# Kernel optimization log

Hardware: AMD Instinct MI355X
Metric: run time of the kernel (lower is better)

The kernel has to match this reference:

```python
import jax, jax.numpy as jnp
import numpy as np

# ---- static config (mirrors init_kwargs) ----
EMBED_DIM = 128
NUM_HEADS = 4
N_SUB = 16       # token grid is N_SUB x N_SUB, seq = N_SUB**2
WINDOW = 4
SHIFT = 2
EPS = 1e-5
NEG_INF = -1e9


def _swin_mask(n_sub, ws, shift):
    """Standard Swin attention mask for shifted windows. [NW, T, T]."""
    img = np.zeros((n_sub, n_sub), np.int32)
    cnt = 0
    for hs in (slice(0, -ws), slice(-ws, -shift), slice(-shift, None)):
        for wsl in (slice(0, -ws), slice(-ws, -shift), slice(-shift, None)):
            img[hs, wsl] = cnt
            cnt += 1
    nw = n_sub // ws
    ids = img.reshape(nw, ws, nw, ws).transpose(0, 2, 1, 3).reshape(nw * nw, ws * ws)
    mask = np.where(ids[:, None, :] != ids[:, :, None], NEG_INF, 0.0).astype(np.float32)
    return jnp.asarray(mask)


MASK = _swin_mask(N_SUB, WINDOW, SHIFT)


def _inorm(v):
    # InstanceNorm2d (affine=False) over spatial dims, per (batch, seq, channel)
    m = v.mean(axis=(-2, -1), keepdims=True)
    var = v.var(axis=(-2, -1), keepdims=True)
    return (v - m) * jax.lax.rsqrt(var + EPS)


def _pw(x, w, b):
    # pointwise (1x1) linear over channel dim of [..., C, H, W]
    return jnp.einsum('...chw,cd->...dhw', x, w) + b[:, None, None]


def _window(x, nw, ws):
    # [B, n_sub, n_sub, C, H, W] -> [B, nw*nw, ws*ws, C, H, W]
    B = x.shape[0]
    C, H, W = x.shape[3:]
    x = x.reshape(B, nw, ws, nw, ws, C, H, W)
    return x.transpose(0, 1, 3, 2, 4, 5, 6, 7).reshape(B, nw * nw, ws * ws, C, H, W)


def _unwindow(x, nw, ws):
    B = x.shape[0]
    C, H, W = x.shape[3:]
    x = x.reshape(B, nw, nw, ws, ws, C, H, W)
    return x.transpose(0, 1, 3, 2, 4, 5, 6, 7).reshape(B, nw * ws, nw * ws, C, H, W)


def _swin_func_attn(v, w_q, b_q, w_k, b_k, w_v, b_v, w_o, b_o):
    B, S, C, H, W = v.shape
    nw = N_SUB // WINDOW
    g = v.reshape(B, N_SUB, N_SUB, C, H, W)
    if SHIFT > 0:
        g = jnp.roll(g, (-SHIFT, -SHIFT), axis=(1, 2))
    q = _window(_pw(g, w_q, b_q), nw, WINDOW)
    k = _window(_pw(g, w_k, b_k), nw, WINDOW)
    val = _window(_pw(g, w_v, b_v), nw, WINDOW)
    d = C // NUM_HEADS
    T = WINDOW * WINDOW
    split = lambda x: x.reshape(B, nw * nw, T, NUM_HEADS, d, H, W)
    q, k, val = split(q), split(k), split(val)
    # integral score: spatial mean of per-head dot products, scaled by sqrt(d)
    scale = 1.0 / (np.sqrt(d) * H * W)
    scores = jnp.einsum('bnthdxy,bnshdxy->bnhts', q, k) * scale
    scores = scores + MASK[None, :, None, :, :]
    attn = jax.nn.softmax(scores, axis=-1)
    o = jnp.einsum('bnhts,bnshdxy->bnthdxy', attn, val)
    o = o.reshape(B, nw * nw, T, C, H, W)
    o = _pw(o, w_o, b_o)
    o = _unwindow(o, nw, WINDOW)
    if SHIFT > 0:
        o = jnp.roll(o, (SHIFT, SHIFT), axis=(1, 2))
    return o.reshape(B, S, C, H, W)


def _mlp(x, w1, b1, w2, b2):
    return _pw(jax.nn.gelu(_pw(x, w1, b1)), w2, b2)


def setup_inputs() -> dict:
    key = jax.random.key(0)
    ks = jax.random.split(key, 8)
    B, S, C, H, W = 8, N_SUB * N_SUB, EMBED_DIM, 16, 16
    p = 0.02
    return {
        'v': jax.random.normal(ks[0], (B, S, C, H, W), jnp.float32),
        'w_q': jax.random.normal(ks[1], (C, C), jnp.float32) * p,
        'b_q': jnp.zeros((C,), jnp.float32),
        'w_k': jax.random.normal(ks[2], (C, C), jnp.float32) * p,
        'b_k': jnp.zeros((C,), jnp.float32),
        'w_v': jax.random.normal(ks[3], (C, C), jnp.float32) * p,
        'b_v': jnp.zeros((C,), jnp.float32),
        'w_o': jax.random.normal(ks[4], (C, C), jnp.float32) * p,
        'b_o': jnp.zeros((C,), jnp.float32),
        'w1': jax.random.normal(ks[5], (C, C), jnp.float32) * p,
        'b1': jnp.zeros((C,), jnp.float32),
        'w2': jax.random.normal(ks[6], (C, C), jnp.float32) * p,
        'b2': jnp.zeros((C,), jnp.float32),
    }


def reference(v, w_q, b_q, w_k, b_k, w_v, b_v, w_o, b_o, w1, b1, w2, b2):
    v = _swin_func_attn(_inorm(v), w_q, b_q, w_k, b_k, w_v, b_v, w_o, b_o) + v
    v = _mlp(_inorm(v), w1, b1, w2, b2) + v
    return v
```

## Files before the change

### kernel.cpp

```cpp
#include <hip/hip_runtime.h>
#include <cstdint>
#include <cstddef>

#define DI __device__ __forceinline__

typedef unsigned short u16;
typedef u16 u16x8 __attribute__((ext_vector_type(8)));
typedef u16 u16x4 __attribute__((ext_vector_type(4)));
typedef float f32x4 __attribute__((ext_vector_type(4)));
typedef __bf16 bf16x8 __attribute__((ext_vector_type(8)));

constexpr float EPSf  = 1e-5f;
constexpr float SCALE = 1.0f / (5.656854249492381f * 256.0f);

DI float bf2f(u16 u) { union { uint32_t i; float f; } v; v.i = ((uint32_t)u) << 16; return v.f; }
DI u16 f2bf(float f) {
    union { float f; uint32_t i; } v; v.f = f;
    uint32_t r = v.i + 0x7fffu + ((v.i >> 16) & 1u);
    return (u16)(r >> 16);
}
DI bf16x8 u2b(u16x8 u) { union { u16x8 a; bf16x8 b; } v; v.a = u; return v.b; }

DI f32x4 MFMA(bf16x8 a, bf16x8 b, f32x4 c) {
    return __builtin_amdgcn_mfma_f32_16x16x32_bf16(a, b, c, 0, 0, 0);
}

DI int region3(int x) { return x < 12 ? 0 : (x < 14 ? 1 : 2); }

DI float gelu_f(float x) {
    float u = 1.5957691216f * x * (1.f + 0.044715f * x * x);
    return x * __builtin_amdgcn_rcpf(1.f + __expf(-u));
}

__global__ __launch_bounds__(256) void kw_prep(
        const float* __restrict__ w_q, const float* __restrict__ w_k,
        const float* __restrict__ w_v, const float* __restrict__ w_o,
        const float* __restrict__ w1,  const float* __restrict__ w2,
        u16* __restrict__ wt) {
    __shared__ float lds[128 * 129];
    const float* W;
    switch (blockIdx.x) {
        case 0: W = w_q; break; case 1: W = w_k; break; case 2: W = w_v; break;
        case 3: W = w_o; break; case 4: W = w1;  break; default: W = w2;  break;
    }
    u16* O = wt + blockIdx.x * 16384;
    int tid = threadIdx.x;
    for (int i = 0; i < 16; i++) {
        int flat = i * 1024 + tid * 4;
        float4 vv = *(const float4*)(W + flat);
        int c = flat >> 7, d = flat & 127;
        lds[c * 129 + d + 0] = vv.x; lds[c * 129 + d + 1] = vv.y;
        lds[c * 129 + d + 2] = vv.z; lds[c * 129 + d + 3] = vv.w;
    }
    __syncthreads();
    for (int i = 0; i < 32; i++) {
        int flat2 = i * 512 + tid * 2;
        int d = flat2 >> 7, c = flat2 & 127;
        u16 a = f2bf(lds[c * 129 + d]);
        u16 b = f2bf(lds[(c + 1) * 129 + d]);
        uint32_t pk = (uint32_t)a | ((uint32_t)b << 16);
        *(uint32_t*)(O + flat2) = pk;
    }
}

__global__ __launch_bounds__(512, 4) void k2_qkv(
        const float* __restrict__ v, const u16* __restrict__ wt,
        const float* __restrict__ b_q, const float* __restrict__ b_k,
        const float* __restrict__ b_v,
        u16* __restrict__ Qg, u16* __restrict__ Kg, u16* __restrict__ Vg) {
    __shared__ __align__(16) u16 Raw[34816];
    __shared__ float red[2][4][128];
    __shared__ float stats[2][128];

    int tid = threadIdx.x;
    int wtk = blockIdx.x;
    int b = wtk >> 8, n = (wtk >> 4) & 15, t = wtk & 15;
    int wi = n >> 2, wj = n & 3, ti = t >> 2, tj = t & 3;
    int si = (wi * 4 + ti + 2) & 15, sj = (wj * 4 + tj + 2) & 15;
    const float* src = v + (size_t)(b * 256 + si * 16 + sj) * 32768;

    int wave = tid >> 6, lane = tid & 63;

    #pragma unroll
    for (int i = 0; i < 16; i++) {
        int c = i * 8 + wave;
        float4 f = *(const float4*)(src + c * 256 + lane * 4);
        u16x4 u; u.x = f2bf(f.x); u.y = f2bf(f.y); u.z = f2bf(f.z); u.w = f2bf(f.w);
        *(u16x4*)&Raw[c * 268 + lane * 4] = u;
    }
    __syncthreads();
    {
        int c = tid & 127, p = tid >> 7;
        float s = 0.f, q = 0.f;
        #pragma unroll
        for (int k = 0; k < 16; k++) {
            u16x4 u = *(const u16x4*)&Raw[c * 268 + p * 64 + k * 4];
            float x0 = bf2f(u.x), x1 = bf2f(u.y), x2 = bf2f(u.z), x3 = bf2f(u.w);
            s += x0 + x1 + x2 + x3;
            q += x0 * x0 + x1 * x1 + x2 * x2 + x3 * x3;
        }
        red[0][p][c] = s; red[1][p][c] = q;
    }
    __syncthreads();
    if (tid < 128) {
        int c = tid;
        float s = red[0][0][c] + red[0][1][c] + red[0][2][c] + red[0][3][c];
        float q = red[1][0][c] + red[1][1][c] + red[1][2][c] + red[1][3][c];
        float mean = s * (1.f / 256.f);
        float var = q * (1.f / 256.f) - mean * mean;
        float a = rsqrtf(var + EPSf);
        stats[0][c] = a; stats[1][c] = -mean * a;
    }
    __syncthreads();

    int lrow = lane & 15, quad = lane >> 4;
    bf16x8 afr[2][4];
    #pragma unroll
    for (int kt = 0; kt < 4; kt++) {
        float sa[8], sb[8];
        #pragma unroll
        for (int j = 0; j < 8; j++) {
            int c = kt * 32 + quad * 8 + j;
            sa[j] = stats[0][c]; sb[j] = stats[1][c];
        }
        #pragma unroll
        for (int mi = 0; mi < 2; mi++) {
            int xy = (wave * 2 + mi) * 16 + lrow;
            u16x8 o;
            #pragma unroll
            for (int j = 0; j < 8; j++) {
                int c = kt * 32 + quad * 8 + j;
                o[j] = f2bf(fmaf(bf2f(Raw[c * 268 + xy]), sa[j], sb[j]));
            }
            afr[mi][kt] = u2b(o);
        }
    }
    __syncthreads();

    u16* WTs  = Raw;
    u16* stgw = Raw + 17408 + wave * 2176;
    for (int w = 0; w < 3; w++) {
        const u16* WTp = wt + w * 16384;
        const float* bias = (w == 0) ? b_q : (w == 1) ? b_k : b_v;
        u16* O = ((w == 0) ? Qg : (w == 1) ? Kg : Vg) + (size_t)wtk * 32768;
        if (w) __syncthreads();
        #pragma unroll
        for (int i = 0; i < 4; i++) {
            int flat = i * 4096 + tid * 8;
            *(u16x8*)&WTs[(flat >> 7) * 136 + (flat & 127)] =
                *(const u16x8*)&WTp[flat];
        }
        __syncthreads();
        f32x4 acc[2][8];
        #pragma unroll
        for (int mi = 0; mi < 2; mi++)
            #pragma unroll
            for (int nt = 0; nt < 8; nt++) acc[mi][nt] = (f32x4){0.f, 0.f, 0.f, 0.f};
        #pragma unroll
        for (int kt = 0; kt < 4; kt++) {
            #pragma unroll
            for (int nt = 0; nt < 8; nt++) {
                bf16x8 bfr = *(const bf16x8*)&WTs[(nt * 16 + lrow) * 136 + kt * 32 + quad * 8];
                acc[0][nt] = MFMA(afr[0][kt], bfr, acc[0][nt]);
                acc[1][nt] = MFMA(afr[1][kt], bfr, acc[1][nt]);
            }
        }
        #pragma unroll
        for (int mi = 0; mi < 2; mi++) {
            int mt = wave * 2 + mi;
            #pragma unroll
            for (int nt = 0; nt < 8; nt++) {
                int d = nt * 16 + lrow;
                float bv = bias[d];
                #pragma unroll
                for (int r = 0; r < 4; r++)
                    stgw[(quad * 4 + r) * 136 + d] = f2bf(acc[mi][nt][r] + bv);
            }
            #pragma unroll
            for (int ro = 0; ro < 4; ro++) {
                int flat = ro * 512 + lane * 8;
                *(u16x8*)&O[mt * 2048 + flat] =
                    *(const u16x8*)&stgw[(flat >> 7) * 136 + (flat & 127)];
            }
        }
    }
}

__global__ __launch_bounds__(1024, 4) void k3_scores(
        const u16* __restrict__ Qg, const u16* __restrict__ Kg,
        float* __restrict__ spart) {
    __shared__ f32x4 red3[3][4][64];
    int tid = threadIdx.x;
    int bid = blockIdx.x;
    int b = bid >> 5, n = (bid >> 1) & 15, half = bid & 1;
    int wtb = (b * 16 + n) * 16;
    int lane = tid & 63, wave = tid >> 6;
    int head = wave & 3, sub = wave >> 2;
    int lrow = lane & 15, quad = lane >> 4;
    int xyb = half * 128 + sub * 32;
    const u16* Qp = Qg + (size_t)(wtb + lrow) * 32768 + (size_t)xyb * 128 + head * 32 + quad * 8;
    const u16* Kp = Kg + (size_t)(wtb + lrow) * 32768 + (size_t)xyb * 128 + head * 32 + quad * 8;
    f32x4 acc = {0.f, 0.f, 0.f, 0.f};
    #pragma unroll 4
    for (int kt = 0; kt < 32; kt++) {
        bf16x8 aq = *(const bf16x8*)(Qp + kt * 128);
        bf16x8 bk = *(const bf16x8*)(Kp + kt * 128);
        acc = MFMA(aq, bk, acc);
    }
    if (sub) red3[sub - 1][head][lane] = acc;
    __syncthreads();
    if (sub == 0) {
        f32x4 a0 = red3[0][head][lane];
        f32x4 a1 = red3[1][head][lane];
        f32x4 a2 = red3[2][head][lane];
        acc = acc + a0 + a1 + a2;
        float* sp = spart + (size_t)(((half * 8 + b) * 16 + n) * 4 + head) * 256;
        for (int r = 0; r < 4; r++) sp[(quad * 4 + r) * 16 + lrow] = acc[r];
    }
}

__global__ __launch_bounds__(512, 4) void k4_attnout(
        const float* __restrict__ v, const u16* __restrict__ Vg,
        const float* __restrict__ spart, const u16* __restrict__ wt,
        const float* __restrict__ b_o, u16* __restrict__ v2) {
    __shared__ __align__(16) u16 Vc[32768];
    __shared__ float attn[4][16][16];
    int tid = threadIdx.x;
    int bid = blockIdx.x;
    int b = bid >> 6, n = (bid >> 2) & 15, qtr = bid & 3;
    int wi = n >> 2, wj = n & 3;
    int wtb = (b * 16 + n) * 16;

    if (tid < 64) {
        int h = tid >> 4, t = tid & 15;
        int it = wi * 4 + (t >> 2) , jt = wj * 4 + (t & 3);
        int rt = region3(it) * 3 + region3(jt);
        const float* sp0 = spart + (size_t)(((0 + b) * 16 + n) * 4 + h) * 256 + t * 16;
        const float* sp1 = spart + (size_t)(((8 + b) * 16 + n) * 4 + h) * 256 + t * 16;
        float vals[16]; float mx = -1e30f;
        for (int s = 0; s < 16; s++) {
            int is = wi * 4 + (s >> 2), js = wj * 4 + (s & 3);
            int rs = region3(is) * 3 + region3(js);
            float sc = (sp0[s] + sp1[s]) * SCALE + (rs == rt ? 0.f : -1e9f);
            vals[s] = sc; mx = fmaxf(mx, sc);
        }
        float sum = 0.f;
        for (int s = 0; s < 16; s++) { vals[s] = __expf(vals[s] - mx); sum += vals[s]; }
        float inv = 1.f / sum;
        for (int s = 0; s < 16; s++) attn[h][t][s] = vals[s] * inv;
    }
    __syncthreads();

    int lane = tid & 63, wave = tid >> 6;
    int lrow = lane & 15, quad = lane >> 4;
    const u16* WoT = wt + 3 * 16384;

    for (int sub = 0; sub < 4; sub++) {
        int xyb = qtr * 64 + sub * 16;
        if (sub) __syncthreads();
        #pragma unroll
        for (int it = 0; it < 8; it++) {
            int flat = (it * 512 + tid) * 8;
            int s = flat >> 11, rem = flat & 2047;
            int xyl = rem >> 7, ch = (rem & 127) >> 3;
            *(u16x8*)&Vc[s * 2048 + xyl * 128 + ((ch ^ (xyl & 7)) << 3)] =
                *(const u16x8*)&Vg[(size_t)(wtb + s) * 32768 + xyb * 128 + rem];
        }
        __syncthreads();
        bf16x8 pa[2][4];
        int t0 = wave * 2, t1 = wave * 2 + 1;
        #pragma unroll
        for (int kt = 0; kt < 4; kt++) {
            float oa[8], ob[8];
            #pragma unroll
            for (int j = 0; j < 8; j++) { oa[j] = 0.f; ob[j] = 0.f; }
            #pragma unroll
            for (int s = 0; s < 16; s++) {
                float a0 = attn[kt][t0][s], a1 = attn[kt][t1][s];
                u16x8 vv = *(const u16x8*)&Vc[s * 2048 + lrow * 128 +
                                              (((kt * 4 + quad) ^ (lrow & 7)) << 3)];
                #pragma unroll
                for (int j = 0; j < 8; j++) {
                    float x = bf2f(vv[j]);
                    oa[j] = fmaf(a0, x, oa[j]);
                    ob[j] = fmaf(a1, x, ob[j]);
                }
            }
            u16x8 ua, ub;
            #pragma unroll
            for (int j = 0; j < 8; j++) { ua[j] = f2bf(oa[j]); ub[j] = f2bf(ob[j]); }
            pa[0][kt] = u2b(ua); pa[1][kt] = u2b(ub);
        }
        __syncthreads();
        f32x4 acc[2][8];
        #pragma unroll
        for (int mi = 0; mi < 2; mi++)
            #pragma unroll
            for (int nt = 0; nt < 8; nt++) acc[mi][nt] = (f32x4){0.f, 0.f, 0.f, 0.f};
        #pragma unroll
        for (int kt = 0; kt < 4; kt++) {
            #pragma unroll
            for (int nt = 0; nt < 8; nt++) {
                bf16x8 bfr = *(const bf16x8*)&WoT[(nt * 16 + lrow) * 128 + kt * 32 + quad * 8];
                acc[0][nt] = MFMA(pa[0][kt], bfr, acc[0][nt]);
                acc[1][nt] = MFMA(pa[1][kt], bfr, acc[1][nt]);
            }
        }
        u16* stgw = Vc + wave * 2176;
        #pragma unroll
        for (int mi = 0; mi < 2; mi++) {
            int mt = wave * 2 + mi;
            int sd = (((wi * 4 + (mt >> 2) + 2) & 15) << 4) | ((wj * 4 + (mt & 3) + 2) & 15);
            size_t tokbase = (size_t)(b * 256 + sd) * 32768;
            #pragma unroll
            for (int nt = 0; nt < 8; nt++) {
                int cc = nt * 16 + lrow;
                float bv = b_o[cc];
                float4 res = *(const float4*)&v[tokbase + (size_t)cc * 256 + xyb + quad * 4];
                stgw[(quad * 4 + 0) * 136 + cc] = f2bf(acc[mi][nt][0] + bv + res.x);
                stgw[(quad * 4 + 1) * 136 + cc] = f2bf(acc[mi][nt][1] + bv + res.y);
                stgw[(quad * 4 + 2) * 136 + cc] = f2bf(acc[mi][nt][2] + bv + res.z);
                stgw[(quad * 4 + 3) * 136 + cc] = f2bf(acc[mi][nt][3] + bv + res.w);
            }
            size_t obase = tokbase + (size_t)xyb * 128;
            #pragma unroll
            for (int ro = 0; ro < 4; ro++) {
                int flat = ro * 512 + lane * 8;
                *(u16x8*)&v2[obase + flat] =
                    *(const u16x8*)&stgw[(flat >> 7) * 136 + (flat & 127)];
            }
        }
    }
}

__global__ __launch_bounds__(512, 4) void k6_mlp(
        const u16* __restrict__ v2, const u16* __restrict__ wt,
        const float* __restrict__ b1, const float* __restrict__ b2,
        float* __restrict__ out) {
    __shared__ __align__(16) u16 Nbuf[256 * 136];
    __shared__ __align__(16) u16 Hbuf[256 * 136];
    __shared__ float red[2][4][128];
    __shared__ float stats[2][128];
    int tid = threadIdx.x;
    size_t tok = blockIdx.x;
    const u16* src = v2 + tok * 32768;

    #pragma unroll
    for (int it = 0; it < 8; it++) {
        int flat = (it * 512 + tid) * 8;
        int xy = flat >> 7, c = flat & 127;
        *(u16x8*)&Nbuf[xy * 136 + c] = *(const u16x8*)&src[flat];
    }
    {
        const u16* W1T = wt + 4 * 16384;
        #pragma unroll
        for (int i = 0; i < 4; i++) {
            int flat = i * 4096 + tid * 8;
            *(u16x8*)&Hbuf[(flat >> 7) * 136 + (flat & 127)] = *(const u16x8*)&W1T[flat];
        }
    }
    __syncthreads();
    {
        int c = tid & 127, p = tid >> 7;
        float s = 0.f, q = 0.f;
        for (int k = 0; k < 64; k++) {
            float x = bf2f(Nbuf[(p * 64 + k) * 136 + c]);
            s += x; q += x * x;
        }
        red[0][p][c] = s; red[1][p][c] = q;
    }
    __syncthreads();
    if (tid < 128) {
        int c = tid;
        float s = red[0][0][c] + red[0][1][c] + red[0][2][c] + red[0][3][c];
        float q = red[1][0][c] + red[1][1][c] + red[1][2][c] + red[1][3][c];
        float mean = s * (1.f / 256.f);
        float var = q * (1.f / 256.f) - mean * mean;
        float a = rsqrtf(var + EPSf);
        stats[0][c] = a; stats[1][c] = -mean * a;
    }
    __syncthreads();

    int wave = tid >> 6, lane = tid & 63;
    int lrow = lane & 15, quad = lane >> 4;
    const u16* W2T = wt + 5 * 16384;

    {
        bf16x8 afr[2][4];
        #pragma unroll
        for (int kt = 0; kt < 4; kt++) {
            float sa[8], sb[8];
            #pragma unroll
            for (int j = 0; j < 8; j++) {
                int c = kt * 32 + quad * 8 + j;
                sa[j] = stats[0][c]; sb[j] = stats[1][c];
            }
            #pragma unroll
            for (int mi = 0; mi < 2; mi++) {
                int mt = wave * 2 + mi;
                u16x8 raw = *(const u16x8*)&Nbuf[(mt * 16 + lrow) * 136 + kt * 32 + quad * 8];
                u16x8 o;
                #pragma unroll
                for (int j = 0; j < 8; j++)
                    o[j] = f2bf(fmaf(bf2f(raw[j]), sa[j], sb[j]));
                afr[mi][kt] = u2b(o);
            }
        }
        f32x4 acc[2][8];
        #pragma unroll
        for (int mi = 0; mi < 2; mi++)
            #pragma unroll
            for (int nt = 0; nt < 8; nt++) acc[mi][nt] = (f32x4){0.f, 0.f, 0.f, 0.f};
        #pragma unroll
        for (int kt = 0; kt < 4; kt++) {
            #pragma unroll
            for (int nt = 0; nt < 8; nt++) {
                bf16x8 bfr = *(const bf16x8*)&Hbuf[(nt * 16 + lrow) * 136 + kt * 32 + quad * 8];
                acc[0][nt] = MFMA(afr[0][kt], bfr, acc[0][nt]);
                acc[1][nt] = MFMA(afr[1][kt], bfr, acc[1][nt]);
            }
        }
        __syncthreads();
        #pragma unroll
        for (int mi = 0; mi < 2; mi++) {
            int mt = wave * 2 + mi;
            #pragma unroll
            for (int nt = 0; nt < 8; nt++) {
                int c = nt * 16 + lrow;
                float bv = b1[c];
                #pragma unroll
                for (int r = 0; r < 4; r++) {
                    float x = acc[mi][nt][r] + bv;
                    Hbuf[(mt * 16 + quad * 4 + r) * 136 + c] = f2bf(gelu_f(x));
                }
            }
        }
    }
    {
        bf16x8 afr[2][4];
        #pragma unroll
        for (int mi = 0; mi < 2; mi++) {
            int mt = wave * 2 + mi;
            #pragma unroll
            for (int kt = 0; kt < 4; kt++)
                afr[mi][kt] = *(const bf16x8*)&Hbuf[(mt * 16 + lrow) * 136 + kt * 32 + quad * 8];
        }
        f32x4 acc[2][8];
        #pragma unroll
        for (int mi = 0; mi < 2; mi++)
            #pragma unroll
            for (int nt = 0; nt < 8; nt++) acc[mi][nt] = (f32x4){0.f, 0.f, 0.f, 0.f};
        #pragma unroll
        for (int kt = 0; kt < 4; kt++) {
            #pragma unroll
            for (int nt = 0; nt < 8; nt++) {
                bf16x8 bfr = *(const bf16x8*)&W2T[(nt * 16 + lrow) * 128 + kt * 32 + quad * 8];
                acc[0][nt] = MFMA(afr[0][kt], bfr, acc[0][nt]);
                acc[1][nt] = MFMA(afr[1][kt], bfr, acc[1][nt]);
            }
        }
        #pragma unroll
        for (int mi = 0; mi < 2; mi++) {
            int mt = wave * 2 + mi;
            #pragma unroll
            for (int nt = 0; nt < 8; nt++) {
                int c = nt * 16 + lrow;
                float bv = b2[c];
                f32x4 o4;
                #pragma unroll
                for (int r = 0; r < 4; r++) {
                    int m = mt * 16 + quad * 4 + r;
                    o4[r] = acc[mi][nt][r] + bv + bf2f(Nbuf[m * 136 + c]);
                }
                *(f32x4*)&out[tok * 32768 + (size_t)c * 256 + mt * 16 + quad * 4] = o4;
            }
        }
    }
}

extern "C" void kernel_launch(void* const* d_in, const int* in_sizes, int n_in,
                              void* d_out, int out_size, void* d_ws, size_t ws_size,
                              hipStream_t stream) {
    const float* v   = (const float*)d_in[0];
    const float* w_q = (const float*)d_in[1];
    const float* b_q = (const float*)d_in[2];
    const float* w_k = (const float*)d_in[3];
    const float* b_k = (const float*)d_in[4];
    const float* w_v = (const float*)d_in[5];
    const float* b_v = (const float*)d_in[6];
    const float* w_o = (const float*)d_in[7];
    const float* b_o = (const float*)d_in[8];
    const float* w1  = (const float*)d_in[9];
    const float* b1  = (const float*)d_in[10];
    const float* w2  = (const float*)d_in[11];
    const float* b2  = (const float*)d_in[12];

    u16*   wt    = (u16*)d_ws;
    float* spart = (float*)((char*)d_ws + 196608);
    u16*   Qg    = (u16*)((char*)d_ws + 1245184);
    u16*   v2    = Qg;
    u16*   Vg    = (u16*)d_out;
    u16*   Kg    = (u16*)d_out + 67108864;
    float* out   = (float*)d_out;

    kw_prep  <<<6,    256,  0, stream>>>(w_q, w_k, w_v, w_o, w1, w2, wt);
    k2_qkv   <<<2048, 512,  0, stream>>>(v, wt, b_q, b_k, b_v, Qg, Kg, Vg);
    k3_scores<<<256,  1024, 0, stream>>>(Qg, Kg, spart);
    k4_attnout<<<512, 512,  0, stream>>>(v, Vg, spart, wt, b_o, v2);
    k6_mlp   <<<2048, 512,  0, stream>>>(v2, wt, b1, b2, out);
}
```

Measured before the change: 1.232 ms.

## Read weights and V directly from global memory, drop LDS staging and syncs

The QKV projection now reads weight fragments straight from global memory instead of staging them in LDS behind barriers. The attention-output kernel loads V rows from global per thread, so the shared V cache and its barriers are gone. The MLP kernel drops its shared activation buffer: statistics come from a register-plus-shuffle reduction over direct global loads, and W1 is read from global. The output GEMMs loop over one M tile at a time to cut accumulator registers. This lowers LDS use and barriers so more blocks can run per CU, at the cost of more global and L2 traffic with less coalesced access.

```diff
diff --git a/kernel.cpp b/kernel.cpp
--- a/kernel.cpp
+++ b/kernel.cpp
@@ -137,20 +137,11 @@
     }
     __syncthreads();
 
-    u16* WTs  = Raw;
-    u16* stgw = Raw + 17408 + wave * 2176;
+    u16* stgw = Raw + wave * 2176;
     for (int w = 0; w < 3; w++) {
         const u16* WTp = wt + w * 16384;
         const float* bias = (w == 0) ? b_q : (w == 1) ? b_k : b_v;
         u16* O = ((w == 0) ? Qg : (w == 1) ? Kg : Vg) + (size_t)wtk * 32768;
-        if (w) __syncthreads();
-        #pragma unroll
-        for (int i = 0; i < 4; i++) {
-            int flat = i * 4096 + tid * 8;
-            *(u16x8*)&WTs[(flat >> 7) * 136 + (flat & 127)] =
-                *(const u16x8*)&WTp[flat];
-        }
-        __syncthreads();
         f32x4 acc[2][8];
         #pragma unroll
         for (int mi = 0; mi < 2; mi++)
@@ -160,7 +151,7 @@
         for (int kt = 0; kt < 4; kt++) {
             #pragma unroll
             for (int nt = 0; nt < 8; nt++) {
-                bf16x8 bfr = *(const bf16x8*)&WTs[(nt * 16 + lrow) * 136 + kt * 32 + quad * 8];
+                bf16x8 bfr = *(const bf16x8*)&WTp[(nt * 16 + lrow) * 128 + kt * 32 + quad * 8];
                 acc[0][nt] = MFMA(afr[0][kt], bfr, acc[0][nt]);
                 acc[1][nt] = MFMA(afr[1][kt], bfr, acc[1][nt]);
             }
@@ -223,8 +214,8 @@
         const float* __restrict__ v, const u16* __restrict__ Vg,
         const float* __restrict__ spart, const u16* __restrict__ wt,
         const float* __restrict__ b_o, u16* __restrict__ v2) {
-    __shared__ __align__(16) u16 Vc[32768];
     __shared__ float attn[4][16][16];
+    __shared__ __align__(16) u16 stg[8 * 2176];
     int tid = threadIdx.x;
     int bid = blockIdx.x;
     int b = bid >> 6, n = (bid >> 2) & 15, qtr = bid & 3;
@@ -254,21 +245,12 @@
     int lane = tid & 63, wave = tid >> 6;
     int lrow = lane & 15, quad = lane >> 4;
     const u16* WoT = wt + 3 * 16384;
+    u16* stgw = stg + wave * 2176;
+    int t0 = wave * 2, t1 = t0 + 1;
 
     for (int sub = 0; sub < 4; sub++) {
         int xyb = qtr * 64 + sub * 16;
-        if (sub) __syncthreads();
-        #pragma unroll
-        for (int it = 0; it < 8; it++) {
-            int flat = (it * 512 + tid) * 8;
-            int s = flat >> 11, rem = flat & 2047;
-            int xyl = rem >> 7, ch = (rem & 127) >> 3;
-            *(u16x8*)&Vc[s * 2048 + xyl * 128 + ((ch ^ (xyl & 7)) << 3)] =
-                *(const u16x8*)&Vg[(size_t)(wtb + s) * 32768 + xyb * 128 + rem];
-        }
-        __syncthreads();
         bf16x8 pa[2][4];
-        int t0 = wave * 2, t1 = wave * 2 + 1;
         #pragma unroll
         for (int kt = 0; kt < 4; kt++) {
             float oa[8], ob[8];
@@ -276,9 +258,9 @@
             for (int j = 0; j < 8; j++) { oa[j] = 0.f; ob[j] = 0.f; }
             #pragma unroll
             for (int s = 0; s < 16; s++) {
+                u16x8 vv = *(const u16x8*)&Vg[(size_t)(wtb + s) * 32768 +
+                                              (size_t)(xyb + lrow) * 128 + kt * 32 + quad * 8];
                 float a0 = attn[kt][t0][s], a1 = attn[kt][t1][s];
-                u16x8 vv = *(const u16x8*)&Vc[s * 2048 + lrow * 128 +
-                                              (((kt * 4 + quad) ^ (lrow & 7)) << 3)];
                 #pragma unroll
                 for (int j = 0; j < 8; j++) {
                     float x = bf2f(vv[j]);
@@ -291,24 +273,19 @@
             for (int j = 0; j < 8; j++) { ua[j] = f2bf(oa[j]); ub[j] = f2bf(ob[j]); }
             pa[0][kt] = u2b(ua); pa[1][kt] = u2b(ub);
         }
-        __syncthreads();
-        f32x4 acc[2][8];
-        #pragma unroll
-        for (int mi = 0; mi < 2; mi++)
-            #pragma unroll
-            for (int nt = 0; nt < 8; nt++) acc[mi][nt] = (f32x4){0.f, 0.f, 0.f, 0.f};
-        #pragma unroll
-        for (int kt = 0; kt < 4; kt++) {
-            #pragma unroll
-            for (int nt = 0; nt < 8; nt++) {
-                bf16x8 bfr = *(const bf16x8*)&WoT[(nt * 16 + lrow) * 128 + kt * 32 + quad * 8];
-                acc[0][nt] = MFMA(pa[0][kt], bfr, acc[0][nt]);
-                acc[1][nt] = MFMA(pa[1][kt], bfr, acc[1][nt]);
-            }
-        }
-        u16* stgw = Vc + wave * 2176;
         #pragma unroll
         for (int mi = 0; mi < 2; mi++) {
+            f32x4 acc[8];
+            #pragma unroll
+            for (int nt = 0; nt < 8; nt++) acc[nt] = (f32x4){0.f, 0.f, 0.f, 0.f};
+            #pragma unroll
+            for (int kt = 0; kt < 4; kt++) {
+                #pragma unroll
+                for (int nt = 0; nt < 8; nt++) {
+                    bf16x8 bfr = *(const bf16x8*)&WoT[(nt * 16 + lrow) * 128 + kt * 32 + quad * 8];
+                    acc[nt] = MFMA(pa[mi][kt], bfr, acc[nt]);
+                }
+            }
             int mt = wave * 2 + mi;
             int sd = (((wi * 4 + (mt >> 2) + 2) & 15) << 4) | ((wj * 4 + (mt & 3) + 2) & 15);
             size_t tokbase = (size_t)(b * 256 + sd) * 32768;
@@ -317,10 +294,10 @@
                 int cc = nt * 16 + lrow;
                 float bv = b_o[cc];
                 float4 res = *(const float4*)&v[tokbase + (size_t)cc * 256 + xyb + quad * 4];
-                stgw[(quad * 4 + 0) * 136 + cc] = f2bf(acc[mi][nt][0] + bv + res.x);
-                stgw[(quad * 4 + 1) * 136 + cc] = f2bf(acc[mi][nt][1] + bv + res.y);
-                stgw[(quad * 4 + 2) * 136 + cc] = f2bf(acc[mi][nt][2] + bv + res.z);
-                stgw[(quad * 4 + 3) * 136 + cc] = f2bf(acc[mi][nt][3] + bv + res.w);
+                stgw[(quad * 4 + 0) * 136 + cc] = f2bf(acc[nt][0] + bv + res.x);
+                stgw[(quad * 4 + 1) * 136 + cc] = f2bf(acc[nt][1] + bv + res.y);
+                stgw[(quad * 4 + 2) * 136 + cc] = f2bf(acc[nt][2] + bv + res.z);
+                stgw[(quad * 4 + 3) * 136 + cc] = f2bf(acc[nt][3] + bv + res.w);
             }
             size_t obase = tokbase + (size_t)xyb * 128;
             #pragma unroll
@@ -337,43 +314,46 @@
         const u16* __restrict__ v2, const u16* __restrict__ wt,
         const float* __restrict__ b1, const float* __restrict__ b2,
         float* __restrict__ out) {
-    __shared__ __align__(16) u16 Nbuf[256 * 136];
     __shared__ __align__(16) u16 Hbuf[256 * 136];
-    __shared__ float red[2][4][128];
+    __shared__ float red[2][8][128];
     __shared__ float stats[2][128];
     int tid = threadIdx.x;
     size_t tok = blockIdx.x;
     const u16* src = v2 + tok * 32768;
-
-    #pragma unroll
-    for (int it = 0; it < 8; it++) {
-        int flat = (it * 512 + tid) * 8;
-        int xy = flat >> 7, c = flat & 127;
-        *(u16x8*)&Nbuf[xy * 136 + c] = *(const u16x8*)&src[flat];
-    }
+    int wave = tid >> 6, lane = tid & 63;
+
     {
-        const u16* W1T = wt + 4 * 16384;
-        #pragma unroll
-        for (int i = 0; i < 4; i++) {
-            int flat = i * 4096 + tid * 8;
-            *(u16x8*)&Hbuf[(flat >> 7) * 136 + (flat & 127)] = *(const u16x8*)&W1T[flat];
-        }
-    }
-    __syncthreads();
-    {
-        int c = tid & 127, p = tid >> 7;
-        float s = 0.f, q = 0.f;
-        for (int k = 0; k < 64; k++) {
-            float x = bf2f(Nbuf[(p * 64 + k) * 136 + c]);
-            s += x; q += x * x;
-        }
-        red[0][p][c] = s; red[1][p][c] = q;
+        float s[8], q[8];
+        #pragma unroll
+        for (int j = 0; j < 8; j++) { s[j] = 0.f; q[j] = 0.f; }
+        #pragma unroll
+        for (int it = 0; it < 8; it++) {
+            u16x8 u = *(const u16x8*)&src[(it * 512 + tid) * 8];
+            #pragma unroll
+            for (int j = 0; j < 8; j++) {
+                float x = bf2f(u[j]);
+                s[j] += x; q[j] += x * x;
+            }
+        }
+        #pragma unroll
+        for (int j = 0; j < 8; j++) {
+            s[j] += __shfl_xor(s[j], 16); s[j] += __shfl_xor(s[j], 32);
+            q[j] += __shfl_xor(q[j], 16); q[j] += __shfl_xor(q[j], 32);
+        }
+        if (lane < 16) {
+            #pragma unroll
+            for (int j = 0; j < 8; j++) {
+                red[0][wave][lane * 8 + j] = s[j];
+                red[1][wave][lane * 8 + j] = q[j];
+            }
+        }
     }
     __syncthreads();
     if (tid < 128) {
         int c = tid;
-        float s = red[0][0][c] + red[0][1][c] + red[0][2][c] + red[0][3][c];
-        float q = red[1][0][c] + red[1][1][c] + red[1][2][c] + red[1][3][c];
+        float s = 0.f, q = 0.f;
+        #pragma unroll
+        for (int w = 0; w < 8; w++) { s += red[0][w][c]; q += red[1][w][c]; }
         float mean = s * (1.f / 256.f);
         float var = q * (1.f / 256.f) - mean * mean;
         float a = rsqrtf(var + EPSf);
@@ -381,99 +361,76 @@
     }
     __syncthreads();
 
-    int wave = tid >> 6, lane = tid & 63;
     int lrow = lane & 15, quad = lane >> 4;
+    const u16* W1T = wt + 4 * 16384;
     const u16* W2T = wt + 5 * 16384;
 
-    {
-        bf16x8 afr[2][4];
+    #pragma unroll
+    for (int mi = 0; mi < 2; mi++) {
+        int mt = wave * 2 + mi;
+        bf16x8 afr[4];
         #pragma unroll
         for (int kt = 0; kt < 4; kt++) {
-            float sa[8], sb[8];
+            u16x8 raw = *(const u16x8*)&src[(mt * 16 + lrow) * 128 + kt * 32 + quad * 8];
+            u16x8 o;
             #pragma unroll
             for (int j = 0; j < 8; j++) {
                 int c = kt * 32 + quad * 8 + j;
-                sa[j] = stats[0][c]; sb[j] = stats[1][c];
-            }
-            #pragma unroll
-            for (int mi = 0; mi < 2; mi++) {
-                int mt = wave * 2 + mi;
-                u16x8 raw = *(const u16x8*)&Nbuf[(mt * 16 + lrow) * 136 + kt * 32 + quad * 8];
-                u16x8 o;
-                #pragma unroll
-                for (int j = 0; j < 8; j++)
-                    o[j] = f2bf(fmaf(bf2f(raw[j]), sa[j], sb[j]));
-                afr[mi][kt] = u2b(o);
-            }
-        }
-        f32x4 acc[2][8];
-        #pragma unroll
-        for (int mi = 0; mi < 2; mi++)
-            #pragma unroll
-            for (int nt = 0; nt < 8; nt++) acc[mi][nt] = (f32x4){0.f, 0.f, 0.f, 0.f};
+                o[j] = f2bf(fmaf(bf2f(raw[j]), stats[0][c], stats[1][c]));
+            }
+            afr[kt] = u2b(o);
+        }
+        f32x4 acc[8];
+        #pragma unroll
+        for (int nt = 0; nt < 8; nt++) acc[nt] = (f32x4){0.f, 0.f, 0.f, 0.f};
         #pragma unroll
         for (int kt = 0; kt < 4; kt++) {
             #pragma unroll
             for (int nt = 0; nt < 8; nt++) {
-                bf16x8 bfr = *(const bf16x8*)&Hbuf[(nt * 16 + lrow) * 136 + kt * 32 + quad * 8];
-                acc[0][nt] = MFMA(afr[0][kt], bfr, acc[0][nt]);
-                acc[1][nt] = MFMA(afr[1][kt], bfr, acc[1][nt]);
-            }
-        }
-        __syncthreads();
-        #pragma unroll
-        for (int mi = 0; mi < 2; mi++) {
-            int mt = wave * 2 + mi;
-            #pragma unroll
-            for (int nt = 0; nt < 8; nt++) {
-                int c = nt * 16 + lrow;
-                float bv = b1[c];
-                #pragma unroll
-                for (int r = 0; r < 4; r++) {
-                    float x = acc[mi][nt][r] + bv;
-                    Hbuf[(mt * 16 + quad * 4 + r) * 136 + c] = f2bf(gelu_f(x));
-                }
-            }
-        }
-    }
-    {
-        bf16x8 afr[2][4];
-        #pragma unroll
-        for (int mi = 0; mi < 2; mi++) {
-            int mt = wave * 2 + mi;
-            #pragma unroll
-            for (int kt = 0; kt < 4; kt++)
-                afr[mi][kt] = *(const bf16x8*)&Hbuf[(mt * 16 + lrow) * 136 + kt * 32 + quad * 8];
-        }
-        f32x4 acc[2][8];
-        #pragma unroll
-        for (int mi = 0; mi < 2; mi++)
-            #pragma unroll
-            for (int nt = 0; nt < 8; nt++) acc[mi][nt] = (f32x4){0.f, 0.f, 0.f, 0.f};
+                bf16x8 bfr = *(const bf16x8*)&W1T[(nt * 16 + lrow) * 128 + kt * 32 + quad * 8];
+                acc[nt] = MFMA(afr[kt], bfr, acc[nt]);
+            }
+        }
+        #pragma unroll
+        for (int nt = 0; nt < 8; nt++) {
+            int c = nt * 16 + lrow;
+            float bv = b1[c];
+            #pragma unroll
+            for (int r = 0; r < 4; r++) {
+                float x = acc[nt][r] + bv;
+                Hbuf[(mt * 16 + quad * 4 + r) * 136 + c] = f2bf(gelu_f(x));
+            }
+        }
+    }
+    #pragma unroll
+    for (int mi = 0; mi < 2; mi++) {
+        int mt = wave * 2 + mi;
+        bf16x8 afr[4];
+        #pragma unroll
+        for (int kt = 0; kt < 4; kt++)
+            afr[kt] = *(const bf16x8*)&Hbuf[(mt * 16 + lrow) * 136 + kt * 32 + quad * 8];
+        f32x4 acc[8];
+        #pragma unroll
+        for (int nt = 0; nt < 8; nt++) acc[nt] = (f32x4){0.f, 0.f, 0.f, 0.f};
         #pragma unroll
         for (int kt = 0; kt < 4; kt++) {
             #pragma unroll
             for (int nt = 0; nt < 8; nt++) {
                 bf16x8 bfr = *(const bf16x8*)&W2T[(nt * 16 + lrow) * 128 + kt * 32 + quad * 8];
-                acc[0][nt] = MFMA(afr[0][kt], bfr, acc[0][nt]);
-                acc[1][nt] = MFMA(afr[1][kt], bfr, acc[1][nt]);
-            }
-        }
-        #pragma unroll
-        for (int mi = 0; mi < 2; mi++) {
-            int mt = wave * 2 + mi;
-            #pragma unroll
-            for (int nt = 0; nt < 8; nt++) {
-                int c = nt * 16 + lrow;
-                float bv = b2[c];
-                f32x4 o4;
-                #pragma unroll
-                for (int r = 0; r < 4; r++) {
-                    int m = mt * 16 + quad * 4 + r;
-                    o4[r] = acc[mi][nt][r] + bv + bf2f(Nbuf[m * 136 + c]);
-                }
-                *(f32x4*)&out[tok * 32768 + (size_t)c * 256 + mt * 16 + quad * 4] = o4;
-            }
+                acc[nt] = MFMA(afr[kt], bfr, acc[nt]);
+            }
+        }
+        #pragma unroll
+        for (int nt = 0; nt < 8; nt++) {
+            int c = nt * 16 + lrow;
+            float bv = b2[c];
+            f32x4 o4;
+            #pragma unroll
+            for (int r = 0; r < 4; r++) {
+                int m = mt * 16 + quad * 4 + r;
+                o4[r] = acc[nt][r] + bv + bf2f(src[m * 128 + c]);
+            }
+            *(f32x4*)&out[tok * 32768 + (size_t)c * 256 + mt * 16 + quad * 4] = o4;
         }
     }
 }
```

Result: slower. 2.043 ms (+65.7%).
